# Performance work log

Hardware: AMD Instinct MI355X
Metric: run time of the kernel (lower is better)

The kernel has to match this reference:

```python
import jax, jax.numpy as jnp
import numpy as np

NEG_INF = jnp.float32(-1e30)  # stand-in for -inf; relu(-inf) == relu(-1e30) == 0


def setup_inputs() -> dict:
    key = jax.random.key(0)
    ks = jax.random.split(key, 8)
    B, S, E = 4, 4096, 512
    query = jax.random.normal(ks[0], (B, S, E), dtype=jnp.float32)
    k_in = jax.random.normal(ks[1], (B, S, E), dtype=jnp.float32)
    v_in = jax.random.normal(ks[2], (B, S, E), dtype=jnp.float32)
    mask = jax.random.randint(ks[3], (B, S, S), 0, 2) > 0  # bool [B,S,S]
    scale = 1.0 / np.sqrt(E)
    W1 = jax.random.uniform(ks[4], (E, E), jnp.float32, -scale, scale)
    b1 = jax.random.uniform(ks[5], (E,), jnp.float32, -scale, scale)
    W2 = jax.random.uniform(ks[6], (E, E), jnp.float32, -scale, scale)
    b2 = jax.random.uniform(ks[7], (E,), jnp.float32, -scale, scale)
    return {"query": query, "key": k_in, "value": v_in, "mask": mask,
            "W1": W1, "b1": b1, "W2": W2, "b2": b2}


def reference(query, key, value, mask, W1, b1, W2, b2):
    # key projection: nn.Linear -> x @ W.T + b
    k = jnp.einsum('bse,fe->bsf', key, W1) + b1
    # raw dot-product correlation scores [B, S, S]
    scores = jnp.einsum('bqe,bke->bqk', query, k)
    # module forces mask[:, :, 0] = True, then fills ~mask with -inf
    m = mask.at[:, :, 0].set(True)
    scores = jnp.where(m, scores, NEG_INF)
    # ReLU instead of softmax (no normalization); dropout is identity in eval
    alpha = jax.nn.relu(scores)
    # value projection then AV matmul
    v = jnp.einsum('bse,fe->bsf', value, W2) + b2
    out = jnp.einsum('bqk,bke->bqe', alpha, v)
    return out
```

## Files before the change

kernel.cpp:

```cpp
#include <hip/hip_runtime.h>
#include <cstdint>


typedef __bf16 bf16x8 __attribute__((ext_vector_type(8)));
typedef float f32x4 __attribute__((ext_vector_type(4)));

__device__ __forceinline__ unsigned short f2bf(float f) {
  unsigned int u = __float_as_uint(f);
  u += 0x7fffu + ((u >> 16) & 1u);
  return (unsigned short)(u >> 16);
}

__device__ __forceinline__ void async_load16(const void* g, void* l) {
  __builtin_amdgcn_global_load_lds(
      (const __attribute__((address_space(1))) unsigned int*)(uintptr_t)g,
      (__attribute__((address_space(3))) unsigned int*)(unsigned int)(uintptr_t)l,
      16, 0, 0);
}

__global__ void cvt3_f32_bf16(const float* __restrict__ i0, const float* __restrict__ i1,
                              const float* __restrict__ i2,
                              unsigned short* __restrict__ o0, unsigned short* __restrict__ o1,
                              unsigned short* __restrict__ o2, int n4) {
  int i = blockIdx.x * blockDim.x + threadIdx.x;
  if (i >= n4) return;
  const float* in = (blockIdx.y == 0) ? i0 : (blockIdx.y == 1) ? i1 : i2;
  unsigned short* out = (blockIdx.y == 0) ? o0 : (blockIdx.y == 1) ? o1 : o2;
  float4 f = ((const float4*)in)[i];
  ushort4 o;
  o.x = f2bf(f.x); o.y = f2bf(f.y); o.z = f2bf(f.z); o.w = f2bf(f.w);
  ((ushort4*)out)[i] = o;
}

__global__ void cvt2_f32_bf16(const float* __restrict__ i0, const float* __restrict__ i1,
                              unsigned short* __restrict__ o0, unsigned short* __restrict__ o1,
                              int n4) {
  int i = blockIdx.x * blockDim.x + threadIdx.x;
  if (i >= n4) return;
  const float* in = (blockIdx.y == 0) ? i0 : i1;
  unsigned short* out = (blockIdx.y == 0) ? o0 : o1;
  float4 f = ((const float4*)in)[i];
  ushort4 o;
  o.x = f2bf(f.x); o.y = f2bf(f.y); o.z = f2bf(f.z); o.w = f2bf(f.w);
  ((ushort4*)out)[i] = o;
}

__global__ void pack_mask(const int* __restrict__ m, unsigned int* __restrict__ bits) {
  const int lane = threadIdx.x & 63;
  const size_t wid = ((size_t)blockIdx.x * blockDim.x + threadIdx.x) >> 6;
  const size_t base = wid * 256;
  unsigned long long bl[4];
#pragma unroll
  for (int c = 0; c < 4; ++c) {
    size_t e = base + (size_t)c * 64 + lane;
    int col = (int)(e & 4095);
    bl[c] = __ballot((m[e] != 0) || (col == 0));
  }
  if (lane < 8)
    bits[base / 32 + lane] = (unsigned int)(bl[lane >> 1] >> ((lane & 1) * 32));
}

__global__ void reduce_split(const float* __restrict__ p, float* __restrict__ out,
                             long long half_elems, int n4) {
  int i = blockIdx.x * blockDim.x + threadIdx.x;
  if (i >= n4) return;
  float4 a = ((const float4*)p)[i];
  float4 b = ((const float4*)(p + half_elems))[i];
  float4 r;
  r.x = a.x + b.x; r.y = a.y + b.y; r.z = a.z + b.z; r.w = a.w + b.w;
  ((float4*)out)[i] = r;
}

template <int EPI>
__global__ void __launch_bounds__(256)
gemm_bt(const unsigned short* __restrict__ A, const unsigned short* __restrict__ B,
        void* __restrict__ Cout, const float* __restrict__ bias,
        const unsigned int* __restrict__ mbits,
        int M, int N, int K,
        long long strA, long long strB, long long strC, long long strM) {
  __shared__ unsigned short sA[128 * 32];
  __shared__ unsigned short sB[128 * 32];

  const int tid  = threadIdx.x;
  const int lane = tid & 63;
  const int wave = tid >> 6;
  const int bz   = blockIdx.z;
  const int tn0  = blockIdx.x * 128;
  const int tm0  = blockIdx.y * 128;

  int bb = bz, kbeg = 0, kend = K;
  if constexpr (EPI == 3) {
    bb = bz & 3;
    kbeg = (bz >> 2) * (K >> 1);
    kend = kbeg + (K >> 1);
  }

  const unsigned short* Ab = A + (size_t)bb * strA;
  const unsigned short* Bb = B + (size_t)bb * strB;

  const int ldrow = lane >> 2;
  const int lcol  = (lane & 3) * 8;
  const int wm = (wave >> 1) * 64;
  const int wn = (wave & 1) * 64;
  const int lr = lane & 15;
  const int lq = lane >> 4;

  f32x4 acc[4][4] = {};

  for (int k0 = kbeg; k0 < kend; k0 += 32) {
#pragma unroll
    for (int l = 0; l < 2; ++l) {
      const int row = wave * 32 + l * 16;
      async_load16(Ab + (size_t)(tm0 + row + ldrow) * K + (k0 + lcol), &sA[row * 32]);
      async_load16(Bb + (size_t)(tn0 + row + ldrow) * K + (k0 + lcol), &sB[row * 32]);
    }
    __syncthreads();

    bf16x8 af[4], bfr[4];
#pragma unroll
    for (int t = 0; t < 4; ++t) {
      af[t]  = *(const bf16x8*)&sA[(wm + t * 16 + lr) * 32 + lq * 8];
      bfr[t] = *(const bf16x8*)&sB[(wn + t * 16 + lr) * 32 + lq * 8];
    }
#pragma unroll
    for (int mt = 0; mt < 4; ++mt)
#pragma unroll
      for (int nt = 0; nt < 4; ++nt)
        acc[mt][nt] = __builtin_amdgcn_mfma_f32_16x16x32_bf16(af[mt], bfr[nt],
                                                              acc[mt][nt], 0, 0, 0);
    __syncthreads();
  }

#pragma unroll
  for (int mt = 0; mt < 4; ++mt) {
#pragma unroll
    for (int r = 0; r < 4; ++r) {
      const int m = tm0 + wm + mt * 16 + lq * 4 + r;
      unsigned long long w64 = 0;
      if constexpr (EPI == 2) {
        w64 = *(const unsigned long long*)&mbits[(size_t)bz * strM +
                                                 (size_t)m * (N >> 5) + ((tn0 + wn) >> 5)];
      }
#pragma unroll
      for (int nt = 0; nt < 4; ++nt) {
        const int n = tn0 + wn + nt * 16 + lr;
        float v = acc[mt][nt][r];
        if constexpr (EPI == 0) {
          v += bias[n];
          ((unsigned short*)Cout)[(size_t)bz * strC + (size_t)m * N + n] = f2bf(v);
        } else if constexpr (EPI == 1) {
          v += bias[m];
          ((unsigned short*)Cout)[(size_t)bz * strC + (size_t)m * N + n] = f2bf(v);
        } else if constexpr (EPI == 2) {
          v = ((w64 >> (nt * 16 + lr)) & 1ull) ? fmaxf(v, 0.f) : 0.f;
          ((unsigned short*)Cout)[(size_t)bz * strC + (size_t)m * N + n] = f2bf(v);
        } else {
          ((float*)Cout)[(size_t)bz * strC + (size_t)m * N + n] = v;
        }
      }
    }
  }
}

extern "C" void kernel_launch(void* const* d_in, const int* in_sizes, int n_in,
                              void* d_out, int out_size, void* d_ws, size_t ws_size,
                              hipStream_t stream) {
  const float* query = (const float*)d_in[0];
  const float* key   = (const float*)d_in[1];
  const float* value = (const float*)d_in[2];
  const int*   mask  = (const int*)d_in[3];
  const float* W1    = (const float*)d_in[4];
  const float* b1    = (const float*)d_in[5];
  const float* W2    = (const float*)d_in[6];
  const float* b2    = (const float*)d_in[7];
  float* out = (float*)d_out;

  constexpr int B = 4, S = 4096, E = 512;
  constexpr long long BSE = (long long)B * S * E;
  constexpr long long SE  = (long long)S * E;
  constexpr long long SS  = (long long)S * S;
  constexpr long long BSS = (long long)B * S * S;
  constexpr long long EE  = (long long)E * E;

  char* ws = (char*)d_ws;
  unsigned short* Qb   = (unsigned short*)ws;  ws += BSE * 2;
  unsigned short* Kb   = (unsigned short*)ws;  ws += BSE * 2;
  unsigned short* Vb   = (unsigned short*)ws;  ws += BSE * 2;
  unsigned short* W1b  = (unsigned short*)ws;  ws += EE * 2;
  unsigned short* W2b  = (unsigned short*)ws;  ws += EE * 2;
  unsigned short* Kp   = (unsigned short*)ws;  ws += BSE * 2;
  unsigned short* Vpt  = (unsigned short*)ws;  ws += BSE * 2;
  unsigned short* alph = (unsigned short*)ws;  ws += BSS * 2;
  unsigned int*   mbit = (unsigned int*)ws;    ws += BSS / 8;
  float*          part = (float*)ws;           ws += BSE * 4 * 2;

  cvt3_f32_bf16<<<dim3(BSE / 1024, 3), 256, 0, stream>>>(
      query, key, value, Qb, Kb, Vb, (int)(BSE / 4));
  cvt2_f32_bf16<<<dim3(EE / 1024, 2), 256, 0, stream>>>(
      W1, W2, W1b, W2b, (int)(EE / 4));

  pack_mask<<<dim3((int)(BSS / 1024)), 256, 0, stream>>>(mask, mbit);

  gemm_bt<0><<<dim3(E / 128, (B * S) / 128, 1), 256, 0, stream>>>(
      Kb, W1b, Kp, b1, nullptr, B * S, E, E, 0, 0, 0, 0);

  gemm_bt<1><<<dim3(S / 128, E / 128, B), 256, 0, stream>>>(
      W2b, Vb, Vpt, b2, nullptr, E, S, E, 0, SE, SE, 0);

  gemm_bt<2><<<dim3(S / 128, S / 128, B), 256, 0, stream>>>(
      Qb, Kp, alph, nullptr, mbit, S, S, E, SE, SE, SS, SS / 32);

  gemm_bt<3><<<dim3(E / 128, S / 128, 2 * B), 256, 0, stream>>>(
      alph, Vpt, part, nullptr, nullptr, S, E, S, SS, SE, SE, 0);

  reduce_split<<<dim3((int)(BSE / 1024)), 256, 0, stream>>>(
      part, out, BSE, (int)(BSE / 4));
}
```

Measured before the change: 744.8 us.

## Double GEMM k-step per barrier and drop split-K reduction for AV matmul

Each GEMM iteration now stages two 32-wide K slices into shared memory before one barrier pair, halving synchronization per K. The AV GEMM no longer splits K across two block groups. It writes fp32 output directly, eliminating the partial buffer and the separate reduction kernel. In exchange, the AV launch has half as many blocks, so each block does a longer serial K loop, and shared memory per block doubles, which may limit occupancy.

```diff
diff --git a/kernel.cpp b/kernel.cpp
--- a/kernel.cpp
+++ b/kernel.cpp
@@ -60,17 +60,6 @@
     bits[base / 32 + lane] = (unsigned int)(bl[lane >> 1] >> ((lane & 1) * 32));
 }
 
-__global__ void reduce_split(const float* __restrict__ p, float* __restrict__ out,
-                             long long half_elems, int n4) {
-  int i = blockIdx.x * blockDim.x + threadIdx.x;
-  if (i >= n4) return;
-  float4 a = ((const float4*)p)[i];
-  float4 b = ((const float4*)(p + half_elems))[i];
-  float4 r;
-  r.x = a.x + b.x; r.y = a.y + b.y; r.z = a.z + b.z; r.w = a.w + b.w;
-  ((float4*)out)[i] = r;
-}
-
 template <int EPI>
 __global__ void __launch_bounds__(256)
 gemm_bt(const unsigned short* __restrict__ A, const unsigned short* __restrict__ B,
@@ -78,8 +67,8 @@
         const unsigned int* __restrict__ mbits,
         int M, int N, int K,
         long long strA, long long strB, long long strC, long long strM) {
-  __shared__ unsigned short sA[128 * 32];
-  __shared__ unsigned short sB[128 * 32];
+  __shared__ unsigned short sA[2 * 128 * 32];
+  __shared__ unsigned short sB[2 * 128 * 32];
 
   const int tid  = threadIdx.x;
   const int lane = tid & 63;
@@ -88,15 +77,8 @@
   const int tn0  = blockIdx.x * 128;
   const int tm0  = blockIdx.y * 128;
 
-  int bb = bz, kbeg = 0, kend = K;
-  if constexpr (EPI == 3) {
-    bb = bz & 3;
-    kbeg = (bz >> 2) * (K >> 1);
-    kend = kbeg + (K >> 1);
-  }
-
-  const unsigned short* Ab = A + (size_t)bb * strA;
-  const unsigned short* Bb = B + (size_t)bb * strB;
+  const unsigned short* Ab = A + (size_t)bz * strA;
+  const unsigned short* Bb = B + (size_t)bz * strB;
 
   const int ldrow = lane >> 2;
   const int lcol  = (lane & 3) * 8;
@@ -107,27 +89,34 @@
 
   f32x4 acc[4][4] = {};
 
-  for (int k0 = kbeg; k0 < kend; k0 += 32) {
-#pragma unroll
-    for (int l = 0; l < 2; ++l) {
-      const int row = wave * 32 + l * 16;
-      async_load16(Ab + (size_t)(tm0 + row + ldrow) * K + (k0 + lcol), &sA[row * 32]);
-      async_load16(Bb + (size_t)(tn0 + row + ldrow) * K + (k0 + lcol), &sB[row * 32]);
+  for (int k0 = 0; k0 < K; k0 += 64) {
+#pragma unroll
+    for (int g = 0; g < 2; ++g)
+#pragma unroll
+      for (int l = 0; l < 2; ++l) {
+        const int row = wave * 32 + l * 16;
+        async_load16(Ab + (size_t)(tm0 + row + ldrow) * K + (k0 + g * 32 + lcol),
+                     &sA[g * 4096 + row * 32]);
+        async_load16(Bb + (size_t)(tn0 + row + ldrow) * K + (k0 + g * 32 + lcol),
+                     &sB[g * 4096 + row * 32]);
+      }
+    __syncthreads();
+
+#pragma unroll
+    for (int g = 0; g < 2; ++g) {
+      bf16x8 af[4], bfr[4];
+#pragma unroll
+      for (int t = 0; t < 4; ++t) {
+        af[t]  = *(const bf16x8*)&sA[g * 4096 + (wm + t * 16 + lr) * 32 + lq * 8];
+        bfr[t] = *(const bf16x8*)&sB[g * 4096 + (wn + t * 16 + lr) * 32 + lq * 8];
+      }
+#pragma unroll
+      for (int mt = 0; mt < 4; ++mt)
+#pragma unroll
+        for (int nt = 0; nt < 4; ++nt)
+          acc[mt][nt] = __builtin_amdgcn_mfma_f32_16x16x32_bf16(af[mt], bfr[nt],
+                                                                acc[mt][nt], 0, 0, 0);
     }
-    __syncthreads();
-
-    bf16x8 af[4], bfr[4];
-#pragma unroll
-    for (int t = 0; t < 4; ++t) {
-      af[t]  = *(const bf16x8*)&sA[(wm + t * 16 + lr) * 32 + lq * 8];
-      bfr[t] = *(const bf16x8*)&sB[(wn + t * 16 + lr) * 32 + lq * 8];
-    }
-#pragma unroll
-    for (int mt = 0; mt < 4; ++mt)
-#pragma unroll
-      for (int nt = 0; nt < 4; ++nt)
-        acc[mt][nt] = __builtin_amdgcn_mfma_f32_16x16x32_bf16(af[mt], bfr[nt],
-                                                              acc[mt][nt], 0, 0, 0);
     __syncthreads();
   }
 
@@ -192,7 +181,6 @@
   unsigned short* Vpt  = (unsigned short*)ws;  ws += BSE * 2;
   unsigned short* alph = (unsigned short*)ws;  ws += BSS * 2;
   unsigned int*   mbit = (unsigned int*)ws;    ws += BSS / 8;
-  float*          part = (float*)ws;           ws += BSE * 4 * 2;
 
   cvt3_f32_bf16<<<dim3(BSE / 1024, 3), 256, 0, stream>>>(
       query, key, value, Qb, Kb, Vb, (int)(BSE / 4));
@@ -210,9 +198,6 @@
   gemm_bt<2><<<dim3(S / 128, S / 128, B), 256, 0, stream>>>(
       Qb, Kp, alph, nullptr, mbit, S, S, E, SE, SE, SS, SS / 32);
 
-  gemm_bt<3><<<dim3(E / 128, S / 128, 2 * B), 256, 0, stream>>>(
-      alph, Vpt, part, nullptr, nullptr, S, E, S, SS, SE, SE, 0);
-
-  reduce_split<<<dim3((int)(BSE / 1024)), 256, 0, stream>>>(
-      part, out, BSE, (int)(BSE / 4));
-}
+  gemm_bt<3><<<dim3(E / 128, S / 128, B), 256, 0, stream>>>(
+      alph, Vpt, out, nullptr, nullptr, S, E, S, SS, SE, SE, 0);
+}
```

Result: faster. 705.9 us (-5.2%).
